# Kernel tuning notes

Measured on AMD Instinct MI355X. Metric: run time of the kernel, lower is better.

## Reference

```python
import jax, jax.numpy as jnp
import numpy as np

THRESHOLD = 0.0
NEG_SLOPE = 0.2   # DGL GATConv leaky_relu negative slope
N, EMB, C = 4096, 2048, 10


def _gat(x, W, a_l, a_r, logm):
    """Dense masked DGL-style GATConv. x:[N,in], W:[in,H*D], a_l/a_r:[H,D],
    logm:[N,N] log edge-multiplicity (-inf where no edge). Returns [N,H,D]."""
    H, D = a_l.shape
    feat = (x @ W).reshape(-1, H, D)                      # [N,H,D]
    el = jnp.einsum('nhd,hd->nh', feat, a_l)              # per-src score
    er = jnp.einsum('nhd,hd->nh', feat, a_r)              # per-dst score
    e = jax.nn.leaky_relu(el[:, None, :] + er[None, :, :], NEG_SLOPE)  # [src,dst,H]
    logits = e + logm[:, :, None]                          # mask + self-loop multiplicity
    alpha = jax.nn.softmax(logits, axis=0)                 # edge softmax over incoming src per dst
    return jnp.einsum('sdh,she->dhe', alpha, feat)         # [N,H,D]


def setup_inputs() -> dict:
    key = jax.random.key(0)
    ks = jax.random.split(key, 12)
    s = lambda fan_in: 1.0 / np.sqrt(fan_in)
    return {
        'deep_features': jax.random.normal(ks[0], (N, EMB), jnp.float32),
        'W1':  jax.random.normal(ks[1], (2048, 1024), jnp.float32) * s(2048),
        'al1': jax.random.normal(ks[2], (1, 1024), jnp.float32) * s(1024),
        'ar1': jax.random.normal(ks[3], (1, 1024), jnp.float32) * s(1024),
        'W2':  jax.random.normal(ks[4], (1024, 2 * 512), jnp.float32) * s(1024),
        'al2': jax.random.normal(ks[5], (2, 512), jnp.float32) * s(512),
        'ar2': jax.random.normal(ks[6], (2, 512), jnp.float32) * s(512),
        'lin1_w': jax.random.normal(ks[7], (2048 + 512, 1024), jnp.float32) * s(2560),
        'lin1_b': jnp.zeros((1024,), jnp.float32),
        'c1_w': jax.random.normal(ks[8], (1024, C), jnp.float32) * s(1024),
        'c1_b': jnp.zeros((C,), jnp.float32),
        'c2_w': jax.random.normal(ks[9], (2048, C), jnp.float32) * s(2048),
        'c2_b': jnp.zeros((C,), jnp.float32),
    }


def reference(deep_features, W1, al1, ar1, W2, al2, ar2,
              lin1_w, lin1_b, c1_w, c1_b, c2_w, c2_b):
    df = deep_features                                     # [N,2048] (ResNet50 features)
    # --- build_graph: cosine similarity threshold graph on detached features ---
    dfs = jax.lax.stop_gradient(df)
    znorm = jnp.linalg.norm(dfs, axis=1, keepdims=True)
    sim = (dfs @ dfs.T) / (znorm @ znorm.T)                # symmetric cosine similarity
    n = df.shape[0]
    # adjacency from threshold (includes self since sim_ii=1>thr) + extra self-loop from dgl.add_self_loop
    mult = (sim > THRESHOLD).astype(df.dtype) + jnp.eye(n, dtype=df.dtype)
    logm = jnp.where(mult > 0, jnp.log(jnp.maximum(mult, 1e-12)), -jnp.inf)
    # --- GAT stack ---
    x = jax.nn.relu(_gat(df, W1, al1, ar1, logm).reshape(n, 1024))
    x = _gat(x, W2, al2, ar2, logm).sum(axis=1)            # sum over 2 heads -> [N,512]
    x = jnp.concatenate([df, x], axis=1)                   # [N,2560]
    x = jax.nn.leaky_relu(x @ lin1_w + lin1_b, 0.01)       # F.leaky_relu default slope
    logits1 = x @ c1_w + c1_b
    logits2 = df @ c2_w + c2_b
    return logits1, logits2
```

## Files before the change

kernel.cpp:

```cpp
#include <hip/hip_runtime.h>
#include <hip/hip_bf16.h>

typedef __hip_bfloat16 bf16;
typedef __attribute__((ext_vector_type(8))) short short8;
typedef __attribute__((ext_vector_type(4))) float f32x4;

#define NN 4096
#define L2E 1.4426950408889634f

__device__ inline float br_sum(float v, float* sd){
  #pragma unroll
  for(int s=32; s>0; s>>=1) v += __shfl_down(v, s, 64);
  int t = threadIdx.x;
  if ((t & 63) == 0) sd[t >> 6] = v;
  __syncthreads();
  float r = (sd[0] + sd[1]) + (sd[2] + sd[3]);
  __syncthreads();
  return r;
}

__device__ inline void gl2lds(const bf16* g, unsigned int* lds){
  __builtin_amdgcn_global_load_lds(
      (const __attribute__((address_space(1))) unsigned int*)g,
      (__attribute__((address_space(3))) unsigned int*)lds, 16, 0, 0);
}

template<int N> __device__ inline void waitvm(){
  if constexpr (N==0)       asm volatile("s_waitcnt vmcnt(0)" ::: "memory");
  else if constexpr (N==4)  asm volatile("s_waitcnt vmcnt(4)" ::: "memory");
  else if constexpr (N==6)  asm volatile("s_waitcnt vmcnt(6)" ::: "memory");
  else if constexpr (N==8)  asm volatile("s_waitcnt vmcnt(8)" ::: "memory");
  else if constexpr (N==12) asm volatile("s_waitcnt vmcnt(12)" ::: "memory");
  else if constexpr (N==18) asm volatile("s_waitcnt vmcnt(18)" ::: "memory");
  else if constexpr (N==24) asm volatile("s_waitcnt vmcnt(24)" ::: "memory");
}
__device__ inline void pipe_barrier(){
  __builtin_amdgcn_s_barrier();
  asm volatile("" ::: "memory");
}

__global__ __launch_bounds__(256)
void prep_all_k(const float* __restrict__ df, const float* __restrict__ W1,
                const float* __restrict__ W2, const float* __restrict__ lw,
                bf16* __restrict__ dfb, bf16* __restrict__ W1tb,
                bf16* __restrict__ W2tb, bf16* __restrict__ lwcat,
                const float* __restrict__ c2w, const float* __restrict__ c2b,
                float* __restrict__ out2)
{
  int b = blockIdx.x, t = threadIdx.x;
  if (b < 4096){
    __shared__ float sd4[4];
    int n = b, k0 = t*8;
    size_t i = (size_t)n*2048 + k0;
    f32x4 v0 = *(const f32x4*)(df + i);
    f32x4 v1 = *(const f32x4*)(df + i + 4);
    short8 s;
    float acc[10] = {};
    #pragma unroll
    for(int q=0;q<4;q++){
      bf16 h0 = __float2bfloat16(v0[q]);
      bf16 h1 = __float2bfloat16(v1[q]);
      s[q]   = *(short*)&h0;
      s[4+q] = *(short*)&h1;
      #pragma unroll
      for(int c=0;c<10;c++){
        acc[c] += v0[q]*c2w[(k0+q)*10 + c] + v1[q]*c2w[(k0+4+q)*10 + c];
      }
    }
    *(short8*)(dfb + i) = s;
    #pragma unroll
    for(int c=0;c<10;c++){
      float r = br_sum(acc[c], sd4);
      if(t==0) out2[n*10 + c] = r + c2b[c];
    }
    return;
  }
  b -= 4096;
  const float* src; bf16* dst; int rb, cb, dstld; bool dup=false;
  if (b < 512){            src=W1; dst=W1tb;  rb=(b>>4)<<6; cb=(b&15)<<6; dstld=2048; }
  else if (b < 768){ b-=512; src=W2; dst=W2tb; rb=(b>>4)<<6; cb=(b&15)<<6; dstld=1024; }
  else { b-=768; src=lw; dst=lwcat; rb=(b>>4)<<6; cb=(b&15)<<6; dstld=3072; dup=(rb>=2048); }
  __shared__ bf16 tile[64][65];
  #pragma unroll
  for(int i=0;i<16;i++){
    int lin=i*256+t, tr=lin>>6, tc=lin&63;
    tile[tr][tc] = __float2bfloat16(src[(size_t)(rb+tr)*1024 + cb+tc]);
  }
  __syncthreads();
  #pragma unroll
  for(int i=0;i<16;i++){
    int lin=i*256+t, tc=lin>>6, tr=lin&63;
    bf16 v = tile[tr][tc];
    dst[(size_t)(cb+tc)*dstld + rb+tr] = v;
    if(dup) dst[(size_t)(cb+tc)*dstld + rb+tr + 512] = v;
  }
}

__device__ __forceinline__
void adj_body(const bf16* __restrict__ A, unsigned int* __restrict__ Cm,
              unsigned int* SH, int idx)
{
  unsigned int* As = SH;
  unsigned int* Bs = SH + 6144;
  const int tid = threadIdx.x;
  int by = (int)((65.0f - sqrtf(4225.0f - 8.0f*(float)idx)) * 0.5f);
  while ((by+1)*(65-(by+1))/2 <= idx) by++;
  while (by*(65-by)/2 > idx) by--;
  int bx = by + (idx - by*(65-by)/2);
  const int bm = by*128, bn = bx*128;
  const int lane = tid&63, wid = tid>>6;
  const int wr = (wid>>1)*64, wc = (wid&1)*64;
  const int quad = lane>>4, mr = lane&15;
  const int L4 = lane>>2;
  const int lsw = (lane&3) ^ ((lane>>3)&3);
  const int qsw4 = ((quad ^ ((mr>>1)&3)) << 2);

  f32x4 acc[4][4];
  #pragma unroll
  for(int i=0;i<4;i++)
    #pragma unroll
    for(int j=0;j<4;j++) acc[i][j] = (f32x4){0.f,0.f,0.f,0.f};

  auto stage = [&](int kb, int p){
    #pragma unroll
    for(int c2=0; c2<2; c2++){
      int row = (wid*2+c2)*16 + L4;
      gl2lds(A + (size_t)(bm+row)*2048 + kb + lsw*8, &As[p*2048 + (wid*2+c2)*256]);
      gl2lds(A + (size_t)(bn+row)*2048 + kb + lsw*8, &Bs[p*2048 + (wid*2+c2)*256]);
    }
  };
  auto compute = [&](int p){
    short8 af[4], bfr[4];
    #pragma unroll
    for(int i=0;i<4;i++)  af[i]  = *(const short8*)&As[p*2048 + (wr + i*16 + mr)*16 + qsw4];
    #pragma unroll
    for(int j=0;j<4;j++)  bfr[j] = *(const short8*)&Bs[p*2048 + (wc + j*16 + mr)*16 + qsw4];
    #pragma unroll
    for(int i=0;i<4;i++)
      #pragma unroll
      for(int j=0;j<4;j++)
        acc[i][j] = __builtin_amdgcn_mfma_f32_16x16x32_bf16(af[i], bfr[j], acc[i][j], 0,0,0);
  };

  stage(0,0); stage(32,1);
  int p = 0;
  #pragma unroll 1
  for(int it=0; it<63; it++){
    waitvm<4>();
    pipe_barrier();
    if (it+2 < 64) stage(32*(it+2), p==0?2:p-1);
    compute(p);
    p = (p==2)?0:p+1;
  }
  waitvm<0>();
  pipe_barrier();
  compute(p);

  #pragma unroll
  for(int i=0;i<4;i++){
    #pragma unroll
    for(int j=0;j<4;j++){
      int cbase = bn + wc + j*16;
      unsigned long long b[4];
      #pragma unroll
      for(int reg=0; reg<4; reg++){
        float v = acc[i][j][reg];
        unsigned long long msk = __ballot(v > 0.f);
        b[reg] = msk;
        if (mr == 0){
          int r = bm + wr + i*16 + quad*4 + reg;
          unsigned int x = (unsigned int)(msk >> (quad*16)) & 0xFFFFu;
          x = (x | (x << 8)) & 0x00FF00FFu;
          x = (x | (x << 4)) & 0x0F0F0F0Fu;
          x = (x | (x << 2)) & 0x33333333u;
          x = (x | (x << 1)) & 0x55555555u;
          if (r >= cbase && r < cbase + 16) x += 1u << (2*(r - cbase));
          Cm[(size_t)r*256 + (cbase>>4)] = x;
        }
      }
      if (bx > by){
        unsigned int x = 0;
        #pragma unroll
        for(int reg=0; reg<4; reg++){
          unsigned long long t = (b[reg] >> mr) & 0x0001000100010001ULL;
          unsigned int f = (unsigned int)((t | (t>>15) | (t>>30) | (t>>45)) & 0xFULL);
          x |= ((f&1u) | ((f&2u)<<7) | ((f&4u)<<14) | ((f&8u)<<21)) << (2*reg);
        }
        if (quad == 0){
          int c = cbase + mr;
          Cm[(size_t)c*256 + ((bm + wr + i*16)>>4)] = x;
        }
      }
    }
  }
}

template<int EPI, int TN, int DUALA, int K, int LDA, int LDBT, int LDC,
         int K1, int LDA2, int WT, int NS>
__device__ __forceinline__
void gemm_body(const bf16* __restrict__ Ag, const bf16* __restrict__ Bt,
               void* __restrict__ Cv, const float* __restrict__ bias,
               const bf16* __restrict__ Ag2, bf16* __restrict__ Ct,
               unsigned int* SH, int bid)
{
  constexpr int NJ  = TN/32;
  constexpr int D   = 2 + TN/64;
  constexpr int NIT = K/32;
  unsigned int* As = SH;
  unsigned int* Bs = SH + NS*2048;
  const int tid = threadIdx.x;
  const int by = 4*(bid&7) + ((bid>>3)&3);
  const int bx = bid>>5;
  const int bm = by*128, bn = bx*TN;
  const int lane = tid&63, wid = tid>>6;
  const int wr = (wid>>1)*64, wc = (wid&1)*(TN/2);
  const int quad = lane>>4, mr = lane&15;
  const int L4 = lane>>2;
  const int lsw = (lane&3) ^ ((lane>>3)&3);
  const int qsw4 = ((quad ^ ((mr>>1)&3)) << 2);

  f32x4 acc[4][NJ];
  #pragma unroll
  for(int i=0;i<4;i++)
    #pragma unroll
    for(int j=0;j<NJ;j++) acc[i][j] = (f32x4){0.f,0.f,0.f,0.f};

  auto stage = [&](int kb, int p){
    #pragma unroll
    for(int c2=0; c2<2; c2++){
      int row = (wid*2+c2)*16 + L4;
      const bf16* ap;
      if (DUALA && kb >= K1) ap = Ag2 + (size_t)(bm+row)*LDA2 + (kb-K1);
      else                   ap = Ag  + (size_t)(bm+row)*LDA  + kb;
      gl2lds(ap + lsw*8, &As[p*2048 + (wid*2+c2)*256]);
    }
    #pragma unroll
    for(int c2=0; c2<TN/64; c2++){
      int row = (wid*(TN/64)+c2)*16 + L4;
      gl2lds(Bt + (size_t)(bn+row)*LDBT + kb + lsw*8,
             &Bs[p*(TN*16) + (wid*(TN/64)+c2)*256]);
    }
  };
  auto compute = [&](int p){
    short8 af[4], bfr[NJ];
    #pragma unroll
    for(int i=0;i<4;i++)
      af[i]  = *(const short8*)&As[p*2048 + (wr + i*16 + mr)*16 + qsw4];
    #pragma unroll
    for(int j=0;j<NJ;j++)
      bfr[j] = *(const short8*)&Bs[p*(TN*16) + (wc + j*16 + mr)*16 + qsw4];
    #pragma unroll
    for(int i=0;i<4;i++)
      #pragma unroll
      for(int j=0;j<NJ;j++)
        acc[i][j] = __builtin_amdgcn_mfma_f32_16x16x32_bf16(af[i], bfr[j], acc[i][j], 0,0,0);
  };

  #pragma unroll
  for(int s=0; s<NS-1; s++) stage(32*s, s);
  int p = 0;
  #pragma unroll 1
  for(int it=0; it<NIT-(NS-1); it++){
    waitvm<(NS-2)*D>();
    pipe_barrier();
    stage(32*(it+NS-1), (p+NS-1)&(NS-1));
    compute(p); p=(p+1)&(NS-1);
  }
  waitvm<0>(); pipe_barrier();
  #pragma unroll 1
  for(int r=0; r<NS-1; r++){ compute(p); p=(p+1)&(NS-1); }

  #pragma unroll
  for(int i=0;i<4;i++){
    #pragma unroll
    for(int j=0;j<NJ;j++){
      #pragma unroll
      for(int reg=0; reg<4; reg++){
        int r = bm + wr + i*16 + quad*4 + reg;
        int c = bn + wc + j*16 + mr;
        float v = acc[i][j][reg];
        if (EPI==1){ ((bf16*)Cv)[(size_t)r*LDC + c] = __float2bfloat16(fmaxf(v,0.f)); }
        if (EPI==2){ ((bf16*)Cv)[(size_t)r*LDC + c] = __float2bfloat16(v); }
        if (EPI==4){ float w = v + bias[c];
                     ((float*)Cv)[(size_t)r*LDC + c] = w > 0.f ? w : 0.01f*w; }
      }
    }
  }

  if (WT){
    __syncthreads();
    bf16* T = (bf16*)SH;
    #pragma unroll
    for(int i=0;i<4;i++)
      #pragma unroll
      for(int j=0;j<NJ;j++)
        #pragma unroll
        for(int reg=0; reg<4; reg++){
          int rl = wr + i*16 + quad*4 + reg;
          int cl = wc + j*16 + mr;
          T[rl*66 + cl] = __float2bfloat16(acc[i][j][reg]);
        }
    __syncthreads();
    #pragma unroll
    for(int w=0; w<TN/4; w++){
      int cl = wid*(TN/4) + w;
      unsigned int v = (unsigned int)(*(unsigned short*)&T[(2*lane)*66 + cl]) |
                       ((unsigned int)(*(unsigned short*)&T[(2*lane+1)*66 + cl]) << 16);
      *(unsigned int*)&Ct[(size_t)(bn+cl)*4096 + bm + 2*lane] = v;
    }
  }
}

template<int EPI, int TN, int DUALA, int K, int LDA, int LDBT, int LDC,
         int K1, int LDA2, int WT, int NS>
__global__ __launch_bounds__(256)
void gemm_k(const bf16* __restrict__ Ag, const bf16* __restrict__ Bt,
            void* __restrict__ Cv, const float* __restrict__ bias,
            const bf16* __restrict__ Ag2, bf16* __restrict__ Ct)
{
  __shared__ unsigned int SH[NS*2048 + NS*TN*16];
  gemm_body<EPI,TN,DUALA,K,LDA,LDBT,LDC,K1,LDA2,WT,NS>(
      Ag, Bt, Cv, bias, Ag2, Ct, SH, blockIdx.x);
}

__global__ __launch_bounds__(256)
void agg2_k(const bf16* __restrict__ P, const bf16* __restrict__ P2,
            const bf16* __restrict__ featT, bf16* __restrict__ x2cat)
{
  __shared__ unsigned int SH[8*2048 + 8*128*16];
  int b = blockIdx.x;
  const bf16* A = (b < 128) ? P : P2;
  const bf16* B = (b < 128) ? featT : featT + (size_t)512*4096;
  bf16* C = (b < 128) ? x2cat : x2cat + 512;
  gemm_body<2,128,0,4096,4096,4096,1024,0,0,0,8>(
      A, B, C, nullptr, nullptr, nullptr, SH, b & 127);
}

__global__ __launch_bounds__(256)
void adjfeat_k(const bf16* __restrict__ dfb, unsigned int* __restrict__ mult2,
               const bf16* __restrict__ W1tb, bf16* __restrict__ featb,
               bf16* __restrict__ featT)
{
  __shared__ unsigned int SH[12288];
  int b = blockIdx.x;
  if (b < 528){
    adj_body(dfb, mult2, SH, b);
  } else {
    gemm_body<2,64,0,2048,2048,2048,1024,0,0,1,4>(
        dfb, W1tb, featb, nullptr, nullptr, featT, SH, b-528);
  }
}

__global__ __launch_bounds__(256)
void elr_k(const bf16* __restrict__ feat, const float* __restrict__ al,
           const float* __restrict__ ar, float* __restrict__ el,
           float* __restrict__ er, int H)
{
  __shared__ float sd[256];
  int n = blockIdx.x, t = threadIdx.x, k0 = t*4;
  unsigned long long sv = *(const unsigned long long*)(feat + (size_t)n*1024 + k0);
  f32x4 av = *(const f32x4*)(al + k0);
  f32x4 rv = *(const f32x4*)(ar + k0);
  float accl = 0.f, accr = 0.f;
  #pragma unroll
  for(int q=0;q<4;q++){
    unsigned short us = (unsigned short)(sv >> (16*q));
    float f = __bfloat162float(*(bf16*)&us);
    accl += f * av[q]; accr += f * rv[q];
  }
  int myh = (H==2) ? (k0 >> 9) : 0;
  for(int h=0; h<H; h++){
    float rl = br_sum(myh==h ? accl : 0.f, sd);
    float rr = br_sum(myh==h ? accr : 0.f, sd);
    if(t==0){ el[h*NN+n] = rl*L2E; er[h*NN+n] = rr*L2E; }
  }
}

__global__ __launch_bounds__(256)
void colp_k(const float* __restrict__ el, const float* __restrict__ er,
            const unsigned int* __restrict__ mult2,
            float* __restrict__ cm, float* __restrict__ cinv,
            bf16* __restrict__ P, bf16* __restrict__ P2)
{
  __shared__ float sd[256];
  int d = blockIdx.x & 4095, hs = blockIdx.x >> 12, t = threadIdx.x;
  el += hs*NN; er += hs*NN; cm += hs*NN; cinv += hs*NN;
  float erd = er[d];
  unsigned int bits = mult2[(size_t)d*256 + t];
  float tv[16];
  float mx = -1e30f;
  const float* ep = el + t*16;
  #pragma unroll
  for(int h=0; h<4; h++){
    f32x4 ev = *(const f32x4*)(ep + h*4);
    #pragma unroll
    for(int q2=0;q2<4;q2++){
      int q = h*4 + q2;
      unsigned int mu = (bits >> (2*q)) & 3u;
      float x = ev[q2] + erd;
      x = fmaxf(x, 0.2f*x);
      if (mu == 2u) x += 1.0f;
      tv[q] = mu ? x : -1e30f;
      mx = fmaxf(mx, tv[q]);
    }
  }
  #pragma unroll
  for(int s=32; s>0; s>>=1) mx = fmaxf(mx, __shfl_down(mx, s, 64));
  if ((t & 63) == 0) sd[t >> 6] = mx;
  __syncthreads();
  float M = fmaxf(fmaxf(sd[0], sd[1]), fmaxf(sd[2], sd[3]));
  __syncthreads();
  float sum = 0.f;
  #pragma unroll
  for(int q=0;q<16;q++) sum += (tv[q] > -1e29f) ? __builtin_exp2f(tv[q]-M) : 0.f;
  sum = br_sum(sum, sd);
  if(t==0){ cm[d] = M; cinv[d] = 1.f/sum; }
  bf16* Pd = (hs == 0) ? P : P2;
  if (Pd){
    float inv = 1.f/sum;
    unsigned int pk[8];
    #pragma unroll
    for(int h=0; h<4; h++){
      #pragma unroll
      for(int q2=0; q2<4; q2++){
        int q = h*4+q2;
        float v = (tv[q] > -1e29f) ? __builtin_exp2f(tv[q]-M)*inv : 0.f;
        bf16 hb = __float2bfloat16(v);
        unsigned short us = *(unsigned short*)&hb;
        if (q2 & 1) pk[h*2 + (q2>>1)] |= ((unsigned int)us << 16);
        else        pk[h*2 + (q2>>1)]  = (unsigned int)us;
      }
    }
    uint4* dst = (uint4*)(Pd + (size_t)d*4096 + t*16);
    dst[0] = *(uint4*)&pk[0];
    dst[1] = *(uint4*)&pk[4];
  }
}

__global__ __launch_bounds__(256)
void pbuild_k(const float* __restrict__ el, const float* __restrict__ er,
              const float* __restrict__ cm, const float* __restrict__ cinv,
              const unsigned int* __restrict__ mult2, bf16* __restrict__ P)
{
  int d = blockIdx.x, t = threadIdx.x;
  const float erd = er[d], md = cm[d], invd = cinv[d];
  unsigned int bits = mult2[(size_t)d*256 + t];
  unsigned int pk[8];
  const float* ep = el + t*16;
  #pragma unroll
  for(int h=0; h<4; h++){
    f32x4 ev = *(const f32x4*)(ep + h*4);
    #pragma unroll
    for(int q2=0; q2<4; q2++){
      int q = h*4+q2;
      unsigned int mu = (bits >> (2*q)) & 3u;
      float x = ev[q2] + erd;
      x = fmaxf(x, 0.2f*x);
      float v = __builtin_exp2f(x + (mu>1u ? 1.0f : 0.0f) - md) * invd;
      v = mu ? v : 0.0f;
      bf16 hb = __float2bfloat16(v);
      unsigned short us = *(unsigned short*)&hb;
      if (q2 & 1) pk[h*2 + (q2>>1)] |= ((unsigned int)us << 16);
      else        pk[h*2 + (q2>>1)]  = (unsigned int)us;
    }
  }
  uint4* dst = (uint4*)(P + (size_t)d*4096 + t*16);
  dst[0] = *(uint4*)&pk[0];
  dst[1] = *(uint4*)&pk[4];
}

__global__ __launch_bounds__(256)
void cls2_k(const float* __restrict__ x3, const float* __restrict__ c1w,
            const float* __restrict__ c1b, float* __restrict__ out)
{
  __shared__ float sd[256];
  int n = blockIdx.x, t = threadIdx.x, k0 = t*4;
  f32x4 xv = *(const f32x4*)(x3 + (size_t)n*1024 + k0);
  float acc[10] = {};
  #pragma unroll
  for(int q=0;q<4;q++){
    #pragma unroll
    for(int c=0;c<10;c++) acc[c] += xv[q] * c1w[(k0+q)*10 + c];
  }
  for(int c=0;c<10;c++){
    float r = br_sum(acc[c], sd);
    if(t==0) out[n*10 + c] = r + c1b[c];
  }
}

extern "C" void kernel_launch(void* const* d_in, const int* in_sizes, int n_in,
                              void* d_out, int out_size, void* d_ws, size_t ws_size,
                              hipStream_t stream) {
  (void)in_sizes; (void)n_in; (void)out_size;
  const float* df  = (const float*)d_in[0];
  const float* W1  = (const float*)d_in[1];
  const float* al1 = (const float*)d_in[2];
  const float* ar1 = (const float*)d_in[3];
  const float* W2  = (const float*)d_in[4];
  const float* al2 = (const float*)d_in[5];
  const float* ar2 = (const float*)d_in[6];
  const float* lw  = (const float*)d_in[7];
  const float* lb  = (const float*)d_in[8];
  const float* c1w = (const float*)d_in[9];
  const float* c1b = (const float*)d_in[10];
  const float* c2w = (const float*)d_in[11];
  const float* c2b = (const float*)d_in[12];
  float* out = (float*)d_out;

  char* Wp = (char*)d_ws;
  bf16* W1tb  = (bf16*)(Wp);
  float* S    = (float*)(Wp);
  bf16* W2tb  = (bf16*)(Wp + ( 4u<<20));
  bf16* lwcat = (bf16*)(Wp + ( 6u<<20));
  unsigned int* mult2 = (unsigned int*)(Wp + (12u<<20));
  bf16* dfb   = (bf16*)(Wp + (16u<<20));
  bf16* featb = (bf16*)(Wp + (32u<<20));
  float* x3   = (float*)(Wp + (32u<<20));
  bf16* featT = (bf16*)(Wp + (40u<<20));
  bf16* x1b   = (bf16*)(Wp + (48u<<20));
  bf16* x2cat = (bf16*)(Wp + (48u<<20));
  bf16* P     = (bf16*)(Wp + (56u<<20));
  bf16* P2    = (bf16*)(Wp + (88u<<20));
  const bool bigws = ws_size >= ((size_t)120 << 20);
  float *el1=S, *er1=S+4096, *el2=S+8192, *er2=S+16384;
  float *m1=S+24576, *i1=S+28672, *m2=S+32768, *i2=S+40960;

  prep_all_k<<<5504,256,0,stream>>>(df, W1, W2, lw, dfb, W1tb, W2tb, lwcat,
                                    c2w, c2b, out + NN*10);

  adjfeat_k<<<1040,256,0,stream>>>(dfb, mult2, W1tb, featb, featT);

  elr_k<<<NN,256,0,stream>>>(featb, al1, ar1, el1, er1, 1);
  colp_k<<<4096,256,0,stream>>>(el1, er1, mult2, m1, i1, P, nullptr);

  gemm_k<1,128,0,4096,4096,4096,1024,0,0,0,8><<<256,256,0,stream>>>(
      P, featT, x1b, nullptr, nullptr, nullptr);

  gemm_k<2,128,0,1024,1024,1024,1024,0,0,1,4><<<256,256,0,stream>>>(
      x1b, W2tb, featb, nullptr, nullptr, featT);

  elr_k<<<NN,256,0,stream>>>(featb, al2, ar2, el2, er2, 2);
  colp_k<<<8192,256,0,stream>>>(el2, er2, mult2, m2, i2, P, bigws ? P2 : nullptr);

  if (bigws){
    agg2_k<<<256,256,0,stream>>>(P, P2, featT, x2cat);
  } else {
    gemm_k<2,64,0,4096,4096,4096,1024,0,0,0,8><<<256,256,0,stream>>>(
        P, featT, x2cat, nullptr, nullptr, nullptr);
    pbuild_k<<<4096,256,0,stream>>>(el2+NN, er2+NN, m2+NN, i2+NN, mult2, P);
    gemm_k<2,64,0,4096,4096,4096,1024,0,0,0,8><<<256,256,0,stream>>>(
        P, featT + (size_t)512*4096, x2cat + 512, nullptr, nullptr, nullptr);
  }

  gemm_k<4,128,1,3072,2048,3072,1024,2048,1024,0,8><<<256,256,0,stream>>>(
      dfb, lwcat, x3, lb, x2cat, nullptr);

  cls2_k<<<4096,256,0,stream>>>(x3, c1w, c1b, out);
}
```

Measured before the change: 446.2 us.

## Fuse attention-score and classifier projections into GEMM epilogues with atomics

The separate elr_k kernels are removed, and the per-node el/er attention scores are computed inside the feature GEMM epilogues through shuffle reductions and atomicAdd. The final cls2_k kernel is removed and the classifier head is fused into the lin1 GEMM epilogue, which accumulates logits atomically into the output. The prep kernel gains extra blocks that zero the score buffers and seed the output with the c1 bias. This drops three launches and the round trips through featb and x3, but adds atomic contention and extra epilogue work, and the result becomes sensitive to summation order.

```diff
diff --git a/kernel.cpp b/kernel.cpp
--- a/kernel.cpp
+++ b/kernel.cpp
@@ -45,7 +45,9 @@
                 bf16* __restrict__ dfb, bf16* __restrict__ W1tb,
                 bf16* __restrict__ W2tb, bf16* __restrict__ lwcat,
                 const float* __restrict__ c2w, const float* __restrict__ c2b,
-                float* __restrict__ out2)
+                float* __restrict__ out2,
+                const float* __restrict__ c1b, float* __restrict__ out1,
+                float* __restrict__ SA, float* __restrict__ SB2)
 {
   int b = blockIdx.x, t = threadIdx.x;
   if (b < 4096){
@@ -73,6 +75,15 @@
       float r = br_sum(acc[c], sd4);
       if(t==0) out2[n*10 + c] = r + c2b[c];
     }
+    return;
+  }
+  if (b >= 5504){
+    int r = (b - 5504)*256 + t;
+    #pragma unroll
+    for(int c=0;c<10;c++) out1[r*10 + c] = c1b[c];
+    SA[r] = 0.f; SA[r + 4096] = 0.f;
+    #pragma unroll
+    for(int q=0;q<4;q++) SB2[r + q*4096] = 0.f;
     return;
   }
   b -= 4096;
@@ -196,11 +207,13 @@
 }
 
 template<int EPI, int TN, int DUALA, int K, int LDA, int LDBT, int LDC,
-         int K1, int LDA2, int WT, int NS>
+         int K1, int LDA2, int WT, int NS, int EL>
 __device__ __forceinline__
 void gemm_body(const bf16* __restrict__ Ag, const bf16* __restrict__ Bt,
                void* __restrict__ Cv, const float* __restrict__ bias,
                const bf16* __restrict__ Ag2, bf16* __restrict__ Ct,
+               const float* __restrict__ eA, const float* __restrict__ eB,
+               float* __restrict__ eX, float* __restrict__ eY,
                unsigned int* SH, int bid)
 {
   constexpr int NJ  = TN/32;
@@ -270,19 +283,76 @@
   #pragma unroll 1
   for(int r=0; r<NS-1; r++){ compute(p); p=(p+1)&(NS-1); }
 
-  #pragma unroll
-  for(int i=0;i<4;i++){
-    #pragma unroll
-    for(int j=0;j<NJ;j++){
+  if (EPI==1 || EPI==2 || EPI==4){
+    #pragma unroll
+    for(int i=0;i<4;i++){
+      #pragma unroll
+      for(int j=0;j<NJ;j++){
+        #pragma unroll
+        for(int reg=0; reg<4; reg++){
+          int r = bm + wr + i*16 + quad*4 + reg;
+          int c = bn + wc + j*16 + mr;
+          float v = acc[i][j][reg];
+          if (EPI==1){ ((bf16*)Cv)[(size_t)r*LDC + c] = __float2bfloat16(fmaxf(v,0.f)); }
+          if (EPI==2){ ((bf16*)Cv)[(size_t)r*LDC + c] = __float2bfloat16(v); }
+          if (EPI==4){ float w = v + bias[c];
+                       ((float*)Cv)[(size_t)r*LDC + c] = w > 0.f ? w : 0.01f*w; }
+        }
+      }
+    }
+  }
+
+  if (EPI==5){
+    #pragma unroll
+    for(int i=0;i<4;i++){
       #pragma unroll
       for(int reg=0; reg<4; reg++){
-        int r = bm + wr + i*16 + quad*4 + reg;
-        int c = bn + wc + j*16 + mr;
-        float v = acc[i][j][reg];
-        if (EPI==1){ ((bf16*)Cv)[(size_t)r*LDC + c] = __float2bfloat16(fmaxf(v,0.f)); }
-        if (EPI==2){ ((bf16*)Cv)[(size_t)r*LDC + c] = __float2bfloat16(v); }
-        if (EPI==4){ float w = v + bias[c];
-                     ((float*)Cv)[(size_t)r*LDC + c] = w > 0.f ? w : 0.01f*w; }
+        float lg[10];
+        #pragma unroll
+        for(int cl=0;cl<10;cl++) lg[cl] = 0.f;
+        #pragma unroll
+        for(int j=0;j<NJ;j++){
+          int c = bn + wc + j*16 + mr;
+          float w = acc[i][j][reg] + bias[c];
+          w = w > 0.f ? w : 0.01f*w;
+          #pragma unroll
+          for(int cl=0;cl<10;cl++) lg[cl] += w * eA[c*10 + cl];
+        }
+        #pragma unroll
+        for(int s=1;s<16;s<<=1)
+          #pragma unroll
+          for(int cl=0;cl<10;cl++) lg[cl] += __shfl_xor(lg[cl], s);
+        if (mr == 0){
+          int n = bm + wr + i*16 + quad*4 + reg;
+          #pragma unroll
+          for(int cl=0;cl<10;cl++) atomicAdd(&eX[n*10 + cl], lg[cl]);
+        }
+      }
+    }
+  }
+
+  if (EL){
+    float* elp = eX; float* erp = eY;
+    if (EL==2){ int hh = bn >> 9; elp += hh*NN; erp += hh*NN; }
+    #pragma unroll
+    for(int i=0;i<4;i++){
+      #pragma unroll
+      for(int reg=0; reg<4; reg++){
+        float pl = 0.f, pr = 0.f;
+        #pragma unroll
+        for(int j=0;j<NJ;j++){
+          int c = bn + wc + j*16 + mr;
+          float v = acc[i][j][reg];
+          pl += v * eA[c];
+          pr += v * eB[c];
+        }
+        #pragma unroll
+        for(int s=1;s<16;s<<=1){ pl += __shfl_xor(pl, s); pr += __shfl_xor(pr, s); }
+        if (mr == 0){
+          int n = bm + wr + i*16 + quad*4 + reg;
+          atomicAdd(&elp[n], pl*L2E);
+          atomicAdd(&erp[n], pr*L2E);
+        }
       }
     }
   }
@@ -312,15 +382,17 @@
 }
 
 template<int EPI, int TN, int DUALA, int K, int LDA, int LDBT, int LDC,
-         int K1, int LDA2, int WT, int NS>
+         int K1, int LDA2, int WT, int NS, int EL>
 __global__ __launch_bounds__(256)
 void gemm_k(const bf16* __restrict__ Ag, const bf16* __restrict__ Bt,
             void* __restrict__ Cv, const float* __restrict__ bias,
-            const bf16* __restrict__ Ag2, bf16* __restrict__ Ct)
+            const bf16* __restrict__ Ag2, bf16* __restrict__ Ct,
+            const float* __restrict__ eA, const float* __restrict__ eB,
+            float* __restrict__ eX, float* __restrict__ eY)
 {
   __shared__ unsigned int SH[NS*2048 + NS*TN*16];
-  gemm_body<EPI,TN,DUALA,K,LDA,LDBT,LDC,K1,LDA2,WT,NS>(
-      Ag, Bt, Cv, bias, Ag2, Ct, SH, blockIdx.x);
+  gemm_body<EPI,TN,DUALA,K,LDA,LDBT,LDC,K1,LDA2,WT,NS,EL>(
+      Ag, Bt, Cv, bias, Ag2, Ct, eA, eB, eX, eY, SH, blockIdx.x);
 }
 
 __global__ __launch_bounds__(256)
@@ -332,47 +404,25 @@
   const bf16* A = (b < 128) ? P : P2;
   const bf16* B = (b < 128) ? featT : featT + (size_t)512*4096;
   bf16* C = (b < 128) ? x2cat : x2cat + 512;
-  gemm_body<2,128,0,4096,4096,4096,1024,0,0,0,8>(
-      A, B, C, nullptr, nullptr, nullptr, SH, b & 127);
+  gemm_body<2,128,0,4096,4096,4096,1024,0,0,0,8,0>(
+      A, B, C, nullptr, nullptr, nullptr, nullptr, nullptr, nullptr, nullptr,
+      SH, b & 127);
 }
 
 __global__ __launch_bounds__(256)
 void adjfeat_k(const bf16* __restrict__ dfb, unsigned int* __restrict__ mult2,
-               const bf16* __restrict__ W1tb, bf16* __restrict__ featb,
-               bf16* __restrict__ featT)
+               const bf16* __restrict__ W1tb, bf16* __restrict__ featT,
+               const float* __restrict__ al1, const float* __restrict__ ar1,
+               float* __restrict__ el1, float* __restrict__ er1)
 {
   __shared__ unsigned int SH[12288];
   int b = blockIdx.x;
   if (b < 528){
     adj_body(dfb, mult2, SH, b);
   } else {
-    gemm_body<2,64,0,2048,2048,2048,1024,0,0,1,4>(
-        dfb, W1tb, featb, nullptr, nullptr, featT, SH, b-528);
-  }
-}
-
-__global__ __launch_bounds__(256)
-void elr_k(const bf16* __restrict__ feat, const float* __restrict__ al,
-           const float* __restrict__ ar, float* __restrict__ el,
-           float* __restrict__ er, int H)
-{
-  __shared__ float sd[256];
-  int n = blockIdx.x, t = threadIdx.x, k0 = t*4;
-  unsigned long long sv = *(const unsigned long long*)(feat + (size_t)n*1024 + k0);
-  f32x4 av = *(const f32x4*)(al + k0);
-  f32x4 rv = *(const f32x4*)(ar + k0);
-  float accl = 0.f, accr = 0.f;
-  #pragma unroll
-  for(int q=0;q<4;q++){
-    unsigned short us = (unsigned short)(sv >> (16*q));
-    float f = __bfloat162float(*(bf16*)&us);
-    accl += f * av[q]; accr += f * rv[q];
-  }
-  int myh = (H==2) ? (k0 >> 9) : 0;
-  for(int h=0; h<H; h++){
-    float rl = br_sum(myh==h ? accl : 0.f, sd);
-    float rr = br_sum(myh==h ? accr : 0.f, sd);
-    if(t==0){ el[h*NN+n] = rl*L2E; er[h*NN+n] = rr*L2E; }
+    gemm_body<0,64,0,2048,2048,2048,1024,0,0,1,4,1>(
+        dfb, W1tb, nullptr, nullptr, nullptr, featT, al1, ar1, el1, er1,
+        SH, b-528);
   }
 }
 
@@ -467,25 +517,6 @@
   uint4* dst = (uint4*)(P + (size_t)d*4096 + t*16);
   dst[0] = *(uint4*)&pk[0];
   dst[1] = *(uint4*)&pk[4];
-}
-
-__global__ __launch_bounds__(256)
-void cls2_k(const float* __restrict__ x3, const float* __restrict__ c1w,
-            const float* __restrict__ c1b, float* __restrict__ out)
-{
-  __shared__ float sd[256];
-  int n = blockIdx.x, t = threadIdx.x, k0 = t*4;
-  f32x4 xv = *(const f32x4*)(x3 + (size_t)n*1024 + k0);
-  float acc[10] = {};
-  #pragma unroll
-  for(int q=0;q<4;q++){
-    #pragma unroll
-    for(int c=0;c<10;c++) acc[c] += xv[q] * c1w[(k0+q)*10 + c];
-  }
-  for(int c=0;c<10;c++){
-    float r = br_sum(acc[c], sd);
-    if(t==0) out[n*10 + c] = r + c1b[c];
-  }
 }
 
 extern "C" void kernel_launch(void* const* d_in, const int* in_sizes, int n_in,
@@ -509,51 +540,49 @@
 
   char* Wp = (char*)d_ws;
   bf16* W1tb  = (bf16*)(Wp);
-  float* S    = (float*)(Wp);
   bf16* W2tb  = (bf16*)(Wp + ( 4u<<20));
   bf16* lwcat = (bf16*)(Wp + ( 6u<<20));
   unsigned int* mult2 = (unsigned int*)(Wp + (12u<<20));
   bf16* dfb   = (bf16*)(Wp + (16u<<20));
-  bf16* featb = (bf16*)(Wp + (32u<<20));
-  float* x3   = (float*)(Wp + (32u<<20));
+  float* SB2  = (float*)(Wp + (32u<<20));
   bf16* featT = (bf16*)(Wp + (40u<<20));
+  float* SA   = (float*)(Wp + (48u<<20));
   bf16* x1b   = (bf16*)(Wp + (48u<<20));
   bf16* x2cat = (bf16*)(Wp + (48u<<20));
   bf16* P     = (bf16*)(Wp + (56u<<20));
   bf16* P2    = (bf16*)(Wp + (88u<<20));
   const bool bigws = ws_size >= ((size_t)120 << 20);
-  float *el1=S, *er1=S+4096, *el2=S+8192, *er2=S+16384;
-  float *m1=S+24576, *i1=S+28672, *m2=S+32768, *i2=S+40960;
-
-  prep_all_k<<<5504,256,0,stream>>>(df, W1, W2, lw, dfb, W1tb, W2tb, lwcat,
-                                    c2w, c2b, out + NN*10);
-
-  adjfeat_k<<<1040,256,0,stream>>>(dfb, mult2, W1tb, featb, featT);
-
-  elr_k<<<NN,256,0,stream>>>(featb, al1, ar1, el1, er1, 1);
+  float *el1 = SA,        *er1 = SA + 4096;
+  float *m1  = SA + 8192, *i1  = SA + 12288;
+  float *el2 = SB2,           *er2 = SB2 + 8192;
+  float *m2  = SB2 + 16384,   *i2  = SB2 + 24576;
+
+  prep_all_k<<<5520,256,0,stream>>>(df, W1, W2, lw, dfb, W1tb, W2tb, lwcat,
+                                    c2w, c2b, out + NN*10, c1b, out, SA, SB2);
+
+  adjfeat_k<<<1040,256,0,stream>>>(dfb, mult2, W1tb, featT, al1, ar1, el1, er1);
+
   colp_k<<<4096,256,0,stream>>>(el1, er1, mult2, m1, i1, P, nullptr);
 
-  gemm_k<1,128,0,4096,4096,4096,1024,0,0,0,8><<<256,256,0,stream>>>(
-      P, featT, x1b, nullptr, nullptr, nullptr);
-
-  gemm_k<2,128,0,1024,1024,1024,1024,0,0,1,4><<<256,256,0,stream>>>(
-      x1b, W2tb, featb, nullptr, nullptr, featT);
-
-  elr_k<<<NN,256,0,stream>>>(featb, al2, ar2, el2, er2, 2);
+  gemm_k<1,128,0,4096,4096,4096,1024,0,0,0,8,0><<<256,256,0,stream>>>(
+      P, featT, x1b, nullptr, nullptr, nullptr, nullptr, nullptr, nullptr, nullptr);
+
+  gemm_k<0,128,0,1024,1024,1024,1024,0,0,1,4,2><<<256,256,0,stream>>>(
+      x1b, W2tb, nullptr, nullptr, nullptr, featT, al2, ar2, el2, er2);
+
   colp_k<<<8192,256,0,stream>>>(el2, er2, mult2, m2, i2, P, bigws ? P2 : nullptr);
 
   if (bigws){
     agg2_k<<<256,256,0,stream>>>(P, P2, featT, x2cat);
   } else {
-    gemm_k<2,64,0,4096,4096,4096,1024,0,0,0,8><<<256,256,0,stream>>>(
-        P, featT, x2cat, nullptr, nullptr, nullptr);
+    gemm_k<2,64,0,4096,4096,4096,1024,0,0,0,8,0><<<256,256,0,stream>>>(
+        P, featT, x2cat, nullptr, nullptr, nullptr, nullptr, nullptr, nullptr, nullptr);
     pbuild_k<<<4096,256,0,stream>>>(el2+NN, er2+NN, m2+NN, i2+NN, mult2, P);
-    gemm_k<2,64,0,4096,4096,4096,1024,0,0,0,8><<<256,256,0,stream>>>(
-        P, featT + (size_t)512*4096, x2cat + 512, nullptr, nullptr, nullptr);
-  }
-
-  gemm_k<4,128,1,3072,2048,3072,1024,2048,1024,0,8><<<256,256,0,stream>>>(
-      dfb, lwcat, x3, lb, x2cat, nullptr);
-
-  cls2_k<<<4096,256,0,stream>>>(x3, c1w, c1b, out);
-}
+    gemm_k<2,64,0,4096,4096,4096,1024,0,0,0,8,0><<<256,256,0,stream>>>(
+        P, featT + (size_t)512*4096, x2cat + 512, nullptr, nullptr, nullptr,
+        nullptr, nullptr, nullptr, nullptr);
+  }
+
+  gemm_k<5,128,1,3072,2048,3072,1024,2048,1024,0,8,0><<<256,256,0,stream>>>(
+      dfb, lwcat, nullptr, lb, x2cat, nullptr, c1w, nullptr, out, nullptr);
+}
```

After: 488.6 us. 9.5% more time.
